# Performance work log

Measured on AMD Instinct MI355X. Metric: run time of the kernel, lower is better.

## Reference

```python
import jax, jax.numpy as jnp
import numpy as np


def fwht(x):
    """Unnormalized fast Walsh-Hadamard transform over a 1-D vector (len = power of 2).
    Matches the torch chunk/cat stage ordering (MSB-first butterfly)."""
    n = x.shape[0]
    ll = int(round(np.log2(n)))
    for ii in range(ll):
        x = x.reshape(2 ** ii, 2, -1)
        x = jnp.concatenate([x[:, :1] + x[:, 1:], x[:, :1] - x[:, 1:]], axis=1)
    return x.reshape(n)


@jax.custom_vjp
def fwht_ff(x):
    # mirrors torch FastWalshHadamard.apply: plain FWHT forward,
    # backward = FWHT(grad) / sqrt(n) (as defined in the original autograd Function)
    return fwht(x)

def _fwht_ff_fwd(x):
    scale = jnp.asarray(1.0 / np.sqrt(float(x.shape[0])), x.dtype)
    return fwht(x), scale

def _fwht_ff_bwd(scale, g):
    return (scale * fwht(g),)

fwht_ff.defvjp(_fwht_ff_fwd, _fwht_ff_bwd)


def fastfood(theta, BB, Pi, GG, DD):
    """Fastfood projection of theta (dim dd) to DD dims using fixed vars."""
    LL = BB.shape[0]
    dd = theta.shape[0]
    k = min(dd, LL)  # F.pad with negative pad truncates; replicate that
    xx = jnp.zeros(LL, theta.dtype).at[:k].set(theta[:k])
    m2 = fwht(BB * xx)          # H B x
    m4 = m2[Pi] * GG            # G Pi H B x
    m5 = fwht_ff(m4)            # H G Pi H B x
    divisor = jnp.sqrt(LL * jnp.sum(GG * GG))
    return m5[:DD] / (divisor * np.sqrt(float(DD) / LL))


def _mk_ff_vars(key, DD):
    ll = int(np.ceil(np.log2(DD)))
    LL = 2 ** ll
    k1, k2, k3 = jax.random.split(key, 3)
    BB = jax.random.randint(k1, (LL,), 0, 2).astype(jnp.float32) * 2.0 - 1.0
    Pi = jax.random.permutation(k2, LL).astype(jnp.int32)
    GG = jax.random.normal(k3, (LL,), dtype=jnp.float32)
    return BB, Pi, GG


D_IN, D_HID, D_OUT = 768, 3072, 768
INTRINSIC = 2048
BATCH = 256


def setup_inputs() -> dict:
    key = jax.random.key(0)
    ks = jax.random.split(key, 12)
    x = jax.random.normal(ks[0], (BATCH, D_IN), dtype=jnp.float32)
    # original initializes intrinsic_parameter to zeros; use small randn so the
    # Fastfood path contributes non-trivially to the output for testing
    theta = jax.random.normal(ks[1], (INTRINSIC,), dtype=jnp.float32) * 0.01
    init_W1 = jax.random.normal(ks[2], (D_HID, D_IN), dtype=jnp.float32) * 0.02
    init_b1 = jax.random.normal(ks[3], (D_HID,), dtype=jnp.float32) * 0.02
    init_W2 = jax.random.normal(ks[4], (D_OUT, D_HID), dtype=jnp.float32) * 0.02
    init_b2 = jax.random.normal(ks[5], (D_OUT,), dtype=jnp.float32) * 0.02
    BB_W1, Pi_W1, GG_W1 = _mk_ff_vars(ks[6], D_HID * D_IN)
    BB_b1, Pi_b1, GG_b1 = _mk_ff_vars(ks[7], D_HID)
    BB_W2, Pi_W2, GG_W2 = _mk_ff_vars(ks[8], D_OUT * D_HID)
    BB_b2, Pi_b2, GG_b2 = _mk_ff_vars(ks[9], D_OUT)
    return {
        'x': x, 'theta': theta,
        'init_W1': init_W1, 'init_b1': init_b1, 'init_W2': init_W2, 'init_b2': init_b2,
        'BB_W1': BB_W1, 'Pi_W1': Pi_W1, 'GG_W1': GG_W1,
        'BB_b1': BB_b1, 'Pi_b1': Pi_b1, 'GG_b1': GG_b1,
        'BB_W2': BB_W2, 'Pi_W2': Pi_W2, 'GG_W2': GG_W2,
        'BB_b2': BB_b2, 'Pi_b2': Pi_b2, 'GG_b2': GG_b2,
    }


def reference(x, theta, init_W1, init_b1, init_W2, init_b2,
              BB_W1, Pi_W1, GG_W1, BB_b1, Pi_b1, GG_b1,
              BB_W2, Pi_W2, GG_W2, BB_b2, Pi_b2, GG_b2):
    # param = initial_value + fastfood(theta) for every wrapped parameter
    W1 = init_W1 + fastfood(theta, BB_W1, Pi_W1, GG_W1, init_W1.size).reshape(init_W1.shape)
    b1 = init_b1 + fastfood(theta, BB_b1, Pi_b1, GG_b1, init_b1.size)
    W2 = init_W2 + fastfood(theta, BB_W2, Pi_W2, GG_W2, init_W2.size).reshape(init_W2.shape)
    b2 = init_b2 + fastfood(theta, BB_b2, Pi_b2, GG_b2, init_b2.size)
    # wrapped module forward: Linear -> ReLU -> Linear
    h = jax.nn.relu(x @ W1.T + b1)
    return h @ W2.T + b2
```

## Files before the change

### kernel.cpp

```cpp
#include <hip/hip_runtime.h>
#include <hip/hip_bf16.h>

typedef __attribute__((ext_vector_type(8))) short bf16x8;
typedef __attribute__((ext_vector_type(8))) unsigned short u16x8;
typedef __attribute__((ext_vector_type(4))) float f32x4;

template <int N, int S>
__device__ __forceinline__ void reg_fwht(float* v) {
#pragma unroll
  for (int h = 1; h < N; h <<= 1)
#pragma unroll
    for (int g = 0; g < N; g += 2 * h)
#pragma unroll
      for (int j = 0; j < h; ++j) {
        float a = v[(g + j) * S], b = v[(g + j + h) * S];
        v[(g + j) * S] = a + b;
        v[(g + j + h) * S] = a - b;
      }
}

__device__ __forceinline__ unsigned short f2bf(float f) {
  unsigned u = __float_as_uint(f);
  unsigned r = (u + 0x7fff + ((u >> 16) & 1)) >> 16;
  return (unsigned short)r;
}

__device__ __forceinline__ void lds_fwht(float* s, int n, int tid, int T) {
  for (int h = 1; h < n; h <<= 1) {
    __syncthreads();
    for (int t = tid; t < (n >> 1); t += T) {
      int i0 = ((t & ~(h - 1)) << 1) | (t & (h - 1));
      int i1 = i0 + h;
      float a = s[i0], b = s[i1];
      s[i0] = a + b;
      s[i1] = a - b;
    }
  }
  __syncthreads();
}

__device__ __forceinline__ void fwht2048_block(float w[8], float* pad,
                                               float* dst, int t) {
  reg_fwht<8, 1>(w);
#pragma unroll
  for (int j = 0; j < 8; ++j) {
    int i = t + 256 * j;
    pad[i + 4 * (i >> 5)] = w[j];
  }
  __syncthreads();
  {
    int base = 8 * t + 4 * (t >> 2);
    float4 a = *(float4*)(pad + base);
    float4 b = *(float4*)(pad + base + 4);
    float u[8] = {a.x, a.y, a.z, a.w, b.x, b.y, b.z, b.w};
    reg_fwht<8, 1>(u);
    *(float4*)(pad + base) = make_float4(u[0], u[1], u[2], u[3]);
    *(float4*)(pad + base + 4) = make_float4(u[4], u[5], u[6], u[7]);
  }
  __syncthreads();
  {
    int b0 = (t & 7) + 64 * (t >> 3);
    float u[8];
#pragma unroll
    for (int j = 0; j < 8; ++j) {
      int i = b0 + 8 * j;
      u[j] = pad[i + 4 * (i >> 5)];
    }
    reg_fwht<8, 1>(u);
#pragma unroll
    for (int j = 0; j < 8; ++j) {
      int i = b0 + 8 * j;
      pad[i + 4 * (i >> 5)] = u[j];
    }
  }
  __syncthreads();
#pragma unroll
  for (int g = 0; g < 2; ++g) {
    int b0 = (t & 63) + 256 * ((g << 2) | (t >> 6));
    float u[4];
#pragma unroll
    for (int j = 0; j < 4; ++j) {
      int i = b0 + 64 * j;
      u[j] = pad[i + 4 * (i >> 5)];
    }
    reg_fwht<4, 1>(u);
#pragma unroll
    for (int j = 0; j < 4; ++j) dst[b0 + 64 * j] = u[j];
  }
  __syncthreads();
}

__global__ __launch_bounds__(256) void k_pre(
    const float* __restrict__ theta, const float* __restrict__ BB0,
    const float* __restrict__ BB1, float* __restrict__ m2s,
    const float* __restrict__ x, __hip_bfloat16* __restrict__ xb) {
  __shared__ __align__(16) float pad[2304];
  int b = blockIdx.x, t = threadIdx.x;
  if (b < 2) {
    const float* BB = b ? BB1 : BB0;
    float w[8];
#pragma unroll
    for (int j = 0; j < 8; ++j) {
      int i = t + 256 * j;
      w[j] = BB[i] * theta[i];
    }
    fwht2048_block(w, pad, m2s + b * 2048, t);
  } else {
    int id0 = (b - 2) * 256 + t;
#pragma unroll
    for (int it = 0; it < 2; ++it) {
      int id = id0 + it * 24576;
      float4 xv = ((const float4*)x)[id];
      ushort4 o;
      o.x = f2bf(xv.x);
      o.y = f2bf(xv.y);
      o.z = f2bf(xv.z);
      o.w = f2bf(xv.w);
      ((ushort4*)xb)[id] = o;
    }
  }
}

#define LLW 4194304

__global__ __launch_bounds__(256) void k_front(
    const int* __restrict__ Pi1, const float* __restrict__ GG1,
    const int* __restrict__ Pi2, const float* __restrict__ GG2,
    const float* __restrict__ m2s, unsigned short* __restrict__ m4b,
    float* __restrict__ partial, const float* __restrict__ theta,
    const float* __restrict__ BBb1, const int* __restrict__ Pib1,
    const float* __restrict__ GGb1, const float* __restrict__ ib1,
    float* __restrict__ b1w, const float* __restrict__ BBb2,
    const int* __restrict__ Pib2, const float* __restrict__ GGb2,
    const float* __restrict__ ib2, float* __restrict__ b2w) {
  __shared__ __align__(16) float s[9216];
  __shared__ float red[4];
  int b = blockIdx.x, t = threadIdx.x;

  if (b >= 2) {
    int bb = b - 2;
    int pipe = bb >> 9, chunk = bb & 511;
    const int* Pi = pipe ? Pi2 : Pi1;
    const float* GG = pipe ? GG2 : GG1;
    const float* mm = m2s + pipe * 2048;
    for (int u = t; u < 512; u += 256) ((float4*)s)[u] = ((const float4*)mm)[u];
    __syncthreads();

    long base = (long)chunk * 8192;
    const int4* p4 = (const int4*)(Pi + base);
    const float4* g4 = (const float4*)(GG + base);
    float v[32];
    float lsum = 0.f;
#pragma unroll
    for (int j = 0; j < 8; ++j) {
      int4 p = p4[t + j * 256];
      float4 g = g4[t + j * 256];
      lsum += g.x * g.x + g.y * g.y + g.z * g.z + g.w * g.w;
      v[j * 4 + 0] = s[p.x & 2047] * g.x;
      v[j * 4 + 1] = s[p.y & 2047] * g.y;
      v[j * 4 + 2] = s[p.z & 2047] * g.z;
      v[j * 4 + 3] = s[p.w & 2047] * g.w;
    }
    for (int off = 32; off; off >>= 1) lsum += __shfl_down(lsum, off, 64);
    if ((t & 63) == 0) red[t >> 6] = lsum;

#pragma unroll
    for (int e = 0; e < 4; ++e) reg_fwht<8, 4>(v + e);

    __syncthreads();
    if (t == 0) partial[pipe * 512 + chunk] = red[0] + red[1] + red[2] + red[3];

#pragma unroll
    for (int j = 0; j < 8; ++j) {
      int A = t * 4 + 4 * (t >> 3) + j * 1152;
      *(float4*)(s + A) =
          make_float4(v[j * 4], v[j * 4 + 1], v[j * 4 + 2], v[j * 4 + 3]);
    }
    __syncthreads();
    {
      int b0 = (t & 31) + (t >> 5) * 1024;
      float w[32];
#pragma unroll
      for (int j2 = 0; j2 < 32; ++j2) {
        int i = b0 + j2 * 32;
        w[j2] = s[i + 4 * (i >> 5)];
      }
      reg_fwht<32, 1>(w);
#pragma unroll
      for (int j2 = 0; j2 < 32; ++j2) {
        int i = b0 + j2 * 32;
        s[i + 4 * (i >> 5)] = w[j2];
      }
    }
    __syncthreads();
#pragma unroll
    for (int q = 0; q < 8; ++q) {
      float4 r = *(const float4*)(s + t * 36 + q * 4);
      v[q * 4 + 0] = r.x;
      v[q * 4 + 1] = r.y;
      v[q * 4 + 2] = r.z;
      v[q * 4 + 3] = r.w;
    }
    reg_fwht<32, 1>(v);
    unsigned short* o = m4b + (long)pipe * LLW;
    long a0 = (long)(2 * t) * 8192 + (long)chunk * 16;
#pragma unroll
    for (int q = 0; q < 4; ++q) {
      u16x8 pk;
#pragma unroll
      for (int e = 0; e < 8; ++e) pk[e] = f2bf(v[q * 8 + e]);
      *(u16x8*)(o + a0 + (q >> 1) * 8192 + (q & 1) * 8) = pk;
    }
  } else if (b == 0) {
    float* tabd = s + 6144;
    float w[8];
#pragma unroll
    for (int j = 0; j < 8; ++j) {
      int i = t + 256 * j;
      w[j] = BBb1[i] * theta[i];
    }
    fwht2048_block(w, s, tabd, t);

    float w16[16];
    float lsum = 0.f;
#pragma unroll
    for (int j = 0; j < 16; ++j) {
      int i = t + 256 * j;
      float g = GGb1[i];
      lsum += g * g;
      w16[j] = tabd[Pib1[i] & 2047] * g;
    }
    reg_fwht<16, 1>(w16);
#pragma unroll
    for (int j = 0; j < 16; ++j) {
      int i = t + 256 * j;
      s[i + 4 * (i >> 5)] = w16[j];
    }
    for (int off = 32; off; off >>= 1) lsum += __shfl_down(lsum, off, 64);
    if ((t & 63) == 0) s[4608 + (t >> 6)] = lsum;
    __syncthreads();
    float S = s[4608] + s[4609] + s[4610] + s[4611];
    {
      int base16 = 16 * t + 4 * (t >> 1);
      float u[16];
#pragma unroll
      for (int q = 0; q < 4; ++q) {
        float4 r = *(float4*)(s + base16 + q * 4);
        u[q * 4 + 0] = r.x;
        u[q * 4 + 1] = r.y;
        u[q * 4 + 2] = r.z;
        u[q * 4 + 3] = r.w;
      }
      reg_fwht<16, 1>(u);
#pragma unroll
      for (int q = 0; q < 4; ++q)
        *(float4*)(s + base16 + q * 4) =
            make_float4(u[q * 4], u[q * 4 + 1], u[q * 4 + 2], u[q * 4 + 3]);
    }
    __syncthreads();
    {
      float scale = 1.0f / sqrtf(S * 3072.0f);
      int b0 = (t & 15) + 256 * (t >> 4);
      float u[16];
#pragma unroll
      for (int j = 0; j < 16; ++j) {
        int i = b0 + 16 * j;
        u[j] = s[i + 4 * (i >> 5)];
      }
      reg_fwht<16, 1>(u);
#pragma unroll
      for (int j = 0; j < 16; ++j) {
        int i = b0 + 16 * j;
        if (i < 3072) b1w[i] = ib1[i] + u[j] * scale;
      }
    }
  } else {
    float* tab2 = s;
    float* m42 = s + 1024;
    for (int i = t; i < 1024; i += 256) tab2[i] = BBb2[i] * theta[i];
    lds_fwht(tab2, 1024, t, 256);
    float lsum = 0.f;
    for (int i = t; i < 1024; i += 256) {
      float g = GGb2[i];
      lsum += g * g;
      m42[i] = tab2[Pib2[i] & 1023] * g;
    }
    for (int off = 32; off; off >>= 1) lsum += __shfl_down(lsum, off, 64);
    if ((t & 63) == 0) s[2048 + (t >> 6)] = lsum;
    lds_fwht(m42, 1024, t, 256);
    float S = s[2048] + s[2049] + s[2050] + s[2051];
    float scale = 1.0f / sqrtf(S * 768.0f);
    for (int i = t; i < 768; i += 256) b2w[i] = ib2[i] + m42[i] * scale;
  }
}

__global__ __launch_bounds__(256) void k_f2c(
    const unsigned short* __restrict__ m4b, const float* __restrict__ iW1,
    const float* __restrict__ iW2, const float* __restrict__ partial,
    __hip_bfloat16* __restrict__ W1b, __hip_bfloat16* __restrict__ W2b) {
  __shared__ __align__(16) float s[10480];
  __shared__ float red[4];
  int b = blockIdx.x, t = threadIdx.x;
  int pipe = b >> 9;
  int lb = b & 511;
  int g = ((lb & 7) << 6) | (lb >> 3);
  int l0 = g * 16;
  const unsigned short* mp = m4b + (long)pipe * LLW + (long)g * 8192;
  const float* initW = pipe ? iW2 : iW1;
  unsigned short* outW = (unsigned short*)(pipe ? W2b : W1b);

  {
    float ps = partial[pipe * 512 + t] + partial[pipe * 512 + 256 + t];
    for (int off = 32; off; off >>= 1) ps += __shfl_down(ps, off, 64);
    if ((t & 63) == 0) red[t >> 6] = ps;
  }

#pragma unroll
  for (int q = 0; q < 4; ++q) {
    u16x8 raw = *(const u16x8*)(mp + t * 32 + q * 8);
    int r = 2 * t + (q >> 1), cb = (q & 1) * 8;
    float* dp = s + r * 20 + (r >> 5) * 16 + cb;
    float4 f0, f1v;
    f0.x = __uint_as_float((unsigned)raw[0] << 16);
    f0.y = __uint_as_float((unsigned)raw[1] << 16);
    f0.z = __uint_as_float((unsigned)raw[2] << 16);
    f0.w = __uint_as_float((unsigned)raw[3] << 16);
    f1v.x = __uint_as_float((unsigned)raw[4] << 16);
    f1v.y = __uint_as_float((unsigned)raw[5] << 16);
    f1v.z = __uint_as_float((unsigned)raw[6] << 16);
    f1v.w = __uint_as_float((unsigned)raw[7] << 16);
    *(float4*)dp = f0;
    *(float4*)(dp + 4) = f1v;
  }
  __syncthreads();

  {
    int c = t & 15, rg = t >> 4;
    float w[32];
#pragma unroll
    for (int j = 0; j < 32; ++j) {
      int r = rg * 32 + j;
      w[j] = s[r * 20 + (r >> 5) * 16 + c];
    }
    reg_fwht<32, 1>(w);
#pragma unroll
    for (int j = 0; j < 32; ++j) {
      int r = rg * 32 + j;
      s[r * 20 + (r >> 5) * 16 + c] = w[j];
    }
  }
  __syncthreads();

  {
    int c = t & 15;
    float w[32];
#pragma unroll
    for (int k = 0; k < 2; ++k) {
      int b0 = (t >> 4) * 2 + k;
#pragma unroll
      for (int j4 = 0; j4 < 16; ++j4) {
        int r = b0 + 32 * j4;
        w[k * 16 + j4] = s[r * 20 + (r >> 5) * 16 + c];
      }
      reg_fwht<16, 1>(w + k * 16);
#pragma unroll
      for (int j4 = 0; j4 < 16; ++j4) {
        int r = b0 + 32 * j4;
        s[r * 20 + (r >> 5) * 16 + c] = w[k * 16 + j4];
      }
    }
  }
  __syncthreads();

  float S = red[0] + red[1] + red[2] + red[3];
  float scale = 1.0f / sqrtf(S * 2359296.0f);
#pragma unroll
  for (int u = 0; u < 5; ++u) {
    int idx = t + u * 256;
    if (idx < 1152) {
      int r = idx >> 2, c4 = (idx & 3) * 4;
      const float* sp = s + r * 20 + (r >> 5) * 16 + c4;
      long gi = (long)r * 8192 + l0 + c4;
      float4 iv = *(const float4*)(initW + gi);
      ushort4 pk;
      pk.x = f2bf(iv.x + sp[0] * scale);
      pk.y = f2bf(iv.y + sp[1] * scale);
      pk.z = f2bf(iv.z + sp[2] * scale);
      pk.w = f2bf(iv.w + sp[3] * scale);
      *(ushort4*)(outW + gi) = pk;
    }
  }
}

template <int NACC, int SPLITK, bool RELU, bool OUT_BF16>
__global__ __launch_bounds__(256) void k_gemm(
    const __hip_bfloat16* __restrict__ A, const __hip_bfloat16* __restrict__ B,
    const float* __restrict__ bias, void* __restrict__ C, int M, int N, int K) {
  __shared__ float red[4 * NACC * 320];
  int wave = threadIdx.x >> 6, lane = threadIdx.x & 63;
  int tileid = blockIdx.x * (4 / SPLITK) + wave / SPLITK;
  int sk = wave % SPLITK;
  int ntiles = N / (16 * NACC);
  int mt = tileid / ntiles, nt = tileid % ntiles;
  int ml = lane & 15;
  int q = lane >> 4;
  const short* As = (const short*)A;
  const short* Bs = (const short*)B;
  long arow = (long)(mt * 16 + ml) * K + q * 8;
  int KS = K / SPLITK, k0 = sk * KS;
  f32x4 acc[NACC] = {};
  for (int k = k0; k < k0 + KS; k += 32) {
    bf16x8 av = *(const bf16x8*)(As + arow + k);
#pragma unroll
    for (int a = 0; a < NACC; ++a) {
      int n = nt * 16 * NACC + a * 16 + ml;
      bf16x8 bv = *(const bf16x8*)(Bs + (long)n * K + q * 8 + k);
      acc[a] = __builtin_amdgcn_mfma_f32_16x16x32_bf16(av, bv, acc[a], 0, 0, 0);
    }
  }
#pragma unroll
  for (int a = 0; a < NACC; ++a)
#pragma unroll
    for (int r = 0; r < 4; ++r)
      red[(wave * NACC + a) * 320 + lane * 5 + r] = acc[a][r];
  __syncthreads();
  if (sk == 0) {
#pragma unroll
    for (int a = 0; a < NACC; ++a) {
      int n = nt * 16 * NACC + a * 16 + ml;
      float bv = bias[n];
#pragma unroll
      for (int r = 0; r < 4; ++r) {
        float vv = bv;
#pragma unroll
        for (int j = 0; j < SPLITK; ++j)
          vv += red[((wave + j) * NACC + a) * 320 + lane * 5 + r];
        int mm = mt * 16 + q * 4 + r;
        if (RELU) vv = fmaxf(vv, 0.f);
        if (OUT_BF16)
          ((__hip_bfloat16*)C)[(long)mm * N + n] = __float2bfloat16(vv);
        else
          ((float*)C)[(long)mm * N + n] = vv;
      }
    }
  }
}

#define OFF_PART 0
#define OFF_M2S 4096
#define OFF_M4B (OFF_M2S + 16384)
#define OFF_W1B (OFF_M4B + 2 * LLW * 2)
#define OFF_W2B (OFF_W1B + 4718592)
#define OFF_HB (OFF_W2B + 4718592)
#define OFF_XB (OFF_HB + 1572864)
#define OFF_B1 (OFF_XB + 393216)
#define OFF_B2 (OFF_B1 + 12288)

extern "C" void kernel_launch(void* const* d_in, const int* in_sizes, int n_in,
                              void* d_out, int out_size, void* d_ws,
                              size_t ws_size, hipStream_t stream) {
  const float* x = (const float*)d_in[0];
  const float* theta = (const float*)d_in[1];
  const float* iW1 = (const float*)d_in[2];
  const float* ib1 = (const float*)d_in[3];
  const float* iW2 = (const float*)d_in[4];
  const float* ib2 = (const float*)d_in[5];
  const float* BB_W1 = (const float*)d_in[6];
  const int* Pi_W1 = (const int*)d_in[7];
  const float* GG_W1 = (const float*)d_in[8];
  const float* BB_b1 = (const float*)d_in[9];
  const int* Pi_b1 = (const int*)d_in[10];
  const float* GG_b1 = (const float*)d_in[11];
  const float* BB_W2 = (const float*)d_in[12];
  const int* Pi_W2 = (const int*)d_in[13];
  const float* GG_W2 = (const float*)d_in[14];
  const float* BB_b2 = (const float*)d_in[15];
  const int* Pi_b2 = (const int*)d_in[16];
  const float* GG_b2 = (const float*)d_in[17];

  char* ws = (char*)d_ws;
  float* partial = (float*)(ws + OFF_PART);
  float* m2s = (float*)(ws + OFF_M2S);
  unsigned short* m4b = (unsigned short*)(ws + OFF_M4B);
  __hip_bfloat16* W1b = (__hip_bfloat16*)(ws + OFF_W1B);
  __hip_bfloat16* W2b = (__hip_bfloat16*)(ws + OFF_W2B);
  __hip_bfloat16* hb = (__hip_bfloat16*)(ws + OFF_HB);
  __hip_bfloat16* xb = (__hip_bfloat16*)(ws + OFF_XB);
  float* b1w = (float*)(ws + OFF_B1);
  float* b2w = (float*)(ws + OFF_B2);

  k_pre<<<98, 256, 0, stream>>>(theta, BB_W1, BB_W2, m2s, x, xb);
  k_front<<<1026, 256, 0, stream>>>(Pi_W1, GG_W1, Pi_W2, GG_W2, m2s, m4b,
                                    partial, theta, BB_b1, Pi_b1, GG_b1, ib1,
                                    b1w, BB_b2, Pi_b2, GG_b2, ib2, b2w);
  k_f2c<<<1024, 256, 0, stream>>>(m4b, iW1, iW2, partial, W1b, W2b);
  k_gemm<2, 2, true, true><<<768, 256, 0, stream>>>(xb, W1b, b1w, hb, 256,
                                                    3072, 768);
  k_gemm<1, 4, false, false><<<768, 256, 0, stream>>>(hb, W2b, b2w, d_out, 256,
                                                      768, 3072);
}
```

Before: 217.1 us.

## Drop pre-kernel: recompute first FWHT per block and convert x to bf16 in GEMM

Removes the k_pre launch. Each k_front block now recomputes the 2048-point H·B·theta transform into shared memory itself, after issuing its Pi/GG loads early so they overlap the FWHT. The first GEMM now reads x as fp32 and converts it to bf16 on the fly. This saves a kernel launch and the intermediate xb/m2s buffers, at the cost of redundant FWHT work in every block and extra fp32 A-operand traffic and conversion inside the GEMM loop.

Result: no change. 221.0 us (+1.8%).

```diff
diff --git a/kernel.cpp b/kernel.cpp
--- a/kernel.cpp
+++ b/kernel.cpp
@@ -90,49 +90,19 @@
   __syncthreads();
 }
 
-__global__ __launch_bounds__(256) void k_pre(
-    const float* __restrict__ theta, const float* __restrict__ BB0,
-    const float* __restrict__ BB1, float* __restrict__ m2s,
-    const float* __restrict__ x, __hip_bfloat16* __restrict__ xb) {
-  __shared__ __align__(16) float pad[2304];
-  int b = blockIdx.x, t = threadIdx.x;
-  if (b < 2) {
-    const float* BB = b ? BB1 : BB0;
-    float w[8];
-#pragma unroll
-    for (int j = 0; j < 8; ++j) {
-      int i = t + 256 * j;
-      w[j] = BB[i] * theta[i];
-    }
-    fwht2048_block(w, pad, m2s + b * 2048, t);
-  } else {
-    int id0 = (b - 2) * 256 + t;
-#pragma unroll
-    for (int it = 0; it < 2; ++it) {
-      int id = id0 + it * 24576;
-      float4 xv = ((const float4*)x)[id];
-      ushort4 o;
-      o.x = f2bf(xv.x);
-      o.y = f2bf(xv.y);
-      o.z = f2bf(xv.z);
-      o.w = f2bf(xv.w);
-      ((ushort4*)xb)[id] = o;
-    }
-  }
-}
-
 #define LLW 4194304
 
 __global__ __launch_bounds__(256) void k_front(
     const int* __restrict__ Pi1, const float* __restrict__ GG1,
     const int* __restrict__ Pi2, const float* __restrict__ GG2,
-    const float* __restrict__ m2s, unsigned short* __restrict__ m4b,
-    float* __restrict__ partial, const float* __restrict__ theta,
-    const float* __restrict__ BBb1, const int* __restrict__ Pib1,
-    const float* __restrict__ GGb1, const float* __restrict__ ib1,
-    float* __restrict__ b1w, const float* __restrict__ BBb2,
-    const int* __restrict__ Pib2, const float* __restrict__ GGb2,
-    const float* __restrict__ ib2, float* __restrict__ b2w) {
+    const float* __restrict__ BBW1, const float* __restrict__ BBW2,
+    unsigned short* __restrict__ m4b, float* __restrict__ partial,
+    const float* __restrict__ theta, const float* __restrict__ BBb1,
+    const int* __restrict__ Pib1, const float* __restrict__ GGb1,
+    const float* __restrict__ ib1, float* __restrict__ b1w,
+    const float* __restrict__ BBb2, const int* __restrict__ Pib2,
+    const float* __restrict__ GGb2, const float* __restrict__ ib2,
+    float* __restrict__ b2w) {
   __shared__ __align__(16) float s[9216];
   __shared__ float red[4];
   int b = blockIdx.x, t = threadIdx.x;
@@ -142,24 +112,40 @@
     int pipe = bb >> 9, chunk = bb & 511;
     const int* Pi = pipe ? Pi2 : Pi1;
     const float* GG = pipe ? GG2 : GG1;
-    const float* mm = m2s + pipe * 2048;
-    for (int u = t; u < 512; u += 256) ((float4*)s)[u] = ((const float4*)mm)[u];
-    __syncthreads();
+    const float* BB = pipe ? BBW2 : BBW1;
 
     long base = (long)chunk * 8192;
     const int4* p4 = (const int4*)(Pi + base);
     const float4* g4 = (const float4*)(GG + base);
+    int4 p[8];
+    float4 gg[8];
+#pragma unroll
+    for (int j = 0; j < 8; ++j) {
+      p[j] = p4[t + j * 256];
+      gg[j] = g4[t + j * 256];
+    }
+
+    {
+      float w8[8];
+#pragma unroll
+      for (int j = 0; j < 8; ++j) {
+        int i = t + 256 * j;
+        w8[j] = BB[i] * theta[i];
+      }
+      fwht2048_block(w8, s, s + 2304, t);
+    }
+    const float* tab = s + 2304;
+
     float v[32];
     float lsum = 0.f;
 #pragma unroll
     for (int j = 0; j < 8; ++j) {
-      int4 p = p4[t + j * 256];
-      float4 g = g4[t + j * 256];
-      lsum += g.x * g.x + g.y * g.y + g.z * g.z + g.w * g.w;
-      v[j * 4 + 0] = s[p.x & 2047] * g.x;
-      v[j * 4 + 1] = s[p.y & 2047] * g.y;
-      v[j * 4 + 2] = s[p.z & 2047] * g.z;
-      v[j * 4 + 3] = s[p.w & 2047] * g.w;
+      lsum += gg[j].x * gg[j].x + gg[j].y * gg[j].y + gg[j].z * gg[j].z +
+              gg[j].w * gg[j].w;
+      v[j * 4 + 0] = tab[p[j].x & 2047] * gg[j].x;
+      v[j * 4 + 1] = tab[p[j].y & 2047] * gg[j].y;
+      v[j * 4 + 2] = tab[p[j].z & 2047] * gg[j].z;
+      v[j * 4 + 3] = tab[p[j].w & 2047] * gg[j].w;
     }
     for (int off = 32; off; off >>= 1) lsum += __shfl_down(lsum, off, 64);
     if ((t & 63) == 0) red[t >> 6] = lsum;
@@ -392,9 +378,9 @@
   }
 }
 
-template <int NACC, int SPLITK, bool RELU, bool OUT_BF16>
+template <int NACC, int SPLITK, bool RELU, bool OUT_BF16, bool AF32>
 __global__ __launch_bounds__(256) void k_gemm(
-    const __hip_bfloat16* __restrict__ A, const __hip_bfloat16* __restrict__ B,
+    const void* __restrict__ A, const __hip_bfloat16* __restrict__ B,
     const float* __restrict__ bias, void* __restrict__ C, int M, int N, int K) {
   __shared__ float red[4 * NACC * 320];
   int wave = threadIdx.x >> 6, lane = threadIdx.x & 63;
@@ -404,13 +390,27 @@
   int mt = tileid / ntiles, nt = tileid % ntiles;
   int ml = lane & 15;
   int q = lane >> 4;
-  const short* As = (const short*)A;
   const short* Bs = (const short*)B;
   long arow = (long)(mt * 16 + ml) * K + q * 8;
   int KS = K / SPLITK, k0 = sk * KS;
   f32x4 acc[NACC] = {};
   for (int k = k0; k < k0 + KS; k += 32) {
-    bf16x8 av = *(const bf16x8*)(As + arow + k);
+    bf16x8 av;
+    if (AF32) {
+      const float* Af = (const float*)A + arow + k;
+      float4 a0 = *(const float4*)Af;
+      float4 a1 = *(const float4*)(Af + 4);
+      av[0] = (short)f2bf(a0.x);
+      av[1] = (short)f2bf(a0.y);
+      av[2] = (short)f2bf(a0.z);
+      av[3] = (short)f2bf(a0.w);
+      av[4] = (short)f2bf(a1.x);
+      av[5] = (short)f2bf(a1.y);
+      av[6] = (short)f2bf(a1.z);
+      av[7] = (short)f2bf(a1.w);
+    } else {
+      av = *(const bf16x8*)((const short*)A + arow + k);
+    }
 #pragma unroll
     for (int a = 0; a < NACC; ++a) {
       int n = nt * 16 * NACC + a * 16 + ml;
@@ -447,13 +447,11 @@
 }
 
 #define OFF_PART 0
-#define OFF_M2S 4096
-#define OFF_M4B (OFF_M2S + 16384)
+#define OFF_M4B 4096
 #define OFF_W1B (OFF_M4B + 2 * LLW * 2)
 #define OFF_W2B (OFF_W1B + 4718592)
 #define OFF_HB (OFF_W2B + 4718592)
-#define OFF_XB (OFF_HB + 1572864)
-#define OFF_B1 (OFF_XB + 393216)
+#define OFF_B1 (OFF_HB + 1572864)
 #define OFF_B2 (OFF_B1 + 12288)
 
 extern "C" void kernel_launch(void* const* d_in, const int* in_sizes, int n_in,
@@ -480,22 +478,20 @@
 
   char* ws = (char*)d_ws;
   float* partial = (float*)(ws + OFF_PART);
-  float* m2s = (float*)(ws + OFF_M2S);
   unsigned short* m4b = (unsigned short*)(ws + OFF_M4B);
   __hip_bfloat16* W1b = (__hip_bfloat16*)(ws + OFF_W1B);
   __hip_bfloat16* W2b = (__hip_bfloat16*)(ws + OFF_W2B);
   __hip_bfloat16* hb = (__hip_bfloat16*)(ws + OFF_HB);
-  __hip_bfloat16* xb = (__hip_bfloat16*)(ws + OFF_XB);
   float* b1w = (float*)(ws + OFF_B1);
   float* b2w = (float*)(ws + OFF_B2);
 
-  k_pre<<<98, 256, 0, stream>>>(theta, BB_W1, BB_W2, m2s, x, xb);
-  k_front<<<1026, 256, 0, stream>>>(Pi_W1, GG_W1, Pi_W2, GG_W2, m2s, m4b,
-                                    partial, theta, BB_b1, Pi_b1, GG_b1, ib1,
-                                    b1w, BB_b2, Pi_b2, GG_b2, ib2, b2w);
+  k_front<<<1026, 256, 0, stream>>>(Pi_W1, GG_W1, Pi_W2, GG_W2, BB_W1, BB_W2,
+                                    m4b, partial, theta, BB_b1, Pi_b1, GG_b1,
+                                    ib1, b1w, BB_b2, Pi_b2, GG_b2, ib2, b2w);
   k_f2c<<<1024, 256, 0, stream>>>(m4b, iW1, iW2, partial, W1b, W2b);
-  k_gemm<2, 2, true, true><<<768, 256, 0, stream>>>(xb, W1b, b1w, hb, 256,
-                                                    3072, 768);
-  k_gemm<1, 4, false, false><<<768, 256, 0, stream>>>(hb, W2b, b2w, d_out, 256,
-                                                      768, 3072);
-}
+  k_gemm<2, 2, true, true, true><<<768, 256, 0, stream>>>(x, W1b, b1w, hb, 256,
+                                                          3072, 768);
+  k_gemm<1, 4, false, false, false><<<768, 256, 0, stream>>>(hb, W2b, b2w,
+                                                             d_out, 256, 768,
+                                                             3072);
+}
```
